# Performance work log

Measured on AMD Instinct MI355X. Metric: run time of the kernel, lower is better.

## Reference

```python
import jax, jax.numpy as jnp
import numpy as np

NUM_EMBEDDINGS = 1024
EMBEDDING_DIM = 64
COMMITMENT_COST = 0.25


def setup_inputs() -> dict:
    key = jax.random.key(0)
    k_in, k_w = jax.random.split(key)
    inputs = jax.random.normal(k_in, (32, 64, 32, 32), dtype=jnp.float32)
    # nn.Embedding weight initialized uniform(-1/K, 1/K)
    bound = 1.0 / NUM_EMBEDDINGS
    weight = jax.random.uniform(k_w, (NUM_EMBEDDINGS, EMBEDDING_DIM),
                                dtype=jnp.float32, minval=-bound, maxval=bound)
    return {"inputs": inputs, "weight": weight}


def reference(inputs, weight):
    # Flatten to [N, D] rows in embedding space
    flat = inputs.reshape(-1, EMBEDDING_DIM)  # [N, D]
    distances = (jnp.sum(flat * flat, axis=1, keepdims=True)
                 + jnp.sum(weight * weight, axis=1)
                 - 2.0 * jnp.matmul(flat, weight.T))
    encoding_indices = jnp.argmin(distances, axis=1)  # [N]
    quantized = weight[encoding_indices].reshape(inputs.shape)
    e_latent_loss = jnp.mean((jax.lax.stop_gradient(quantized) - inputs) ** 2)
    q_latent_loss = jnp.mean((quantized - jax.lax.stop_gradient(inputs)) ** 2)
    commitment_loss = COMMITMENT_COST * (q_latent_loss + e_latent_loss)
    # Straight-through estimator
    quantized = inputs + jax.lax.stop_gradient(quantized - inputs)
    return quantized, encoding_indices[:, None], commitment_loss
```

## Files before the change

kernel.cpp:

```cpp
#include <hip/hip_runtime.h>

#define NROWS  32768
#define DIM    64
#define KCODES 1024
#define NELEM  (NROWS * DIM)

__device__ __forceinline__ float np_sumsq64(const float v[64]) {
#pragma clang fp contract(off)
  float r0 = v[0] * v[0];
  float r1 = v[1] * v[1];
  float r2 = v[2] * v[2];
  float r3 = v[3] * v[3];
  float r4 = v[4] * v[4];
  float r5 = v[5] * v[5];
  float r6 = v[6] * v[6];
  float r7 = v[7] * v[7];
#pragma unroll
  for (int i = 8; i < 64; i += 8) {
    r0 += v[i + 0] * v[i + 0];
    r1 += v[i + 1] * v[i + 1];
    r2 += v[i + 2] * v[i + 2];
    r3 += v[i + 3] * v[i + 3];
    r4 += v[i + 4] * v[i + 4];
    r5 += v[i + 5] * v[i + 5];
    r6 += v[i + 6] * v[i + 6];
    r7 += v[i + 7] * v[i + 7];
  }
  return ((r0 + r1) + (r2 + r3)) + ((r4 + r5) + (r6 + r7));
}

__global__ void vq_prep(const float* __restrict__ w, float* __restrict__ se,
                        double* __restrict__ loss) {
  int c = blockIdx.x * 256 + threadIdx.x;
  if (c == 0) *loss = 0.0;
  if (c < KCODES) {
    float v[64];
    const float4* wr = (const float4*)(w + (size_t)c * DIM);
#pragma unroll
    for (int i = 0; i < 16; ++i) {
      float4 t = wr[i];
      v[4 * i + 0] = t.x; v[4 * i + 1] = t.y;
      v[4 * i + 2] = t.z; v[4 * i + 3] = t.w;
    }
    se[c] = np_sumsq64(v);
  }
}

__global__ __launch_bounds__(256) void vq_dist(const float* __restrict__ x,
                                               const float* __restrict__ w,
                                               const float* __restrict__ se,
                                               unsigned long long* __restrict__ keys) {
  const int g = blockIdx.x >> 2;
  const int chunk = blockIdx.x & 3;
  const int row = g * 256 + threadIdx.x;

  float xv[64];
  const float4* xr = (const float4*)(x + (size_t)row * DIM);
#pragma unroll
  for (int i = 0; i < 16; ++i) {
    float4 t = xr[i];
    xv[4 * i + 0] = t.x; xv[4 * i + 1] = t.y;
    xv[4 * i + 2] = t.z; xv[4 * i + 3] = t.w;
  }
  const float sx = np_sumsq64(xv);

  const int c0 = chunk * 256;
  const float4* w4 = (const float4*)w;
  unsigned long long best = 0xFFFFFFFFFFFFFFFFull;

#pragma unroll 2
  for (int j = 0; j < 256; ++j) {
    const int c = c0 + j;
    const float4* wr = w4 + (size_t)c * 16;
    float a0 = 0.f, a1 = 0.f, a2 = 0.f, a3 = 0.f;
#pragma unroll
    for (int i = 0; i < 16; ++i) {
      float4 t = wr[i];
      a0 += t.x * xv[4 * i + 0];
      a1 += t.y * xv[4 * i + 1];
      a2 += t.z * xv[4 * i + 2];
      a3 += t.w * xv[4 * i + 3];
    }
    float dot = (a0 + a1) + (a2 + a3);
    float ad = sx + se[c];
    float d  = ad - 2.0f * dot;
    unsigned long long key =
        ((unsigned long long)__float_as_uint(d) << 32) | (unsigned long long)c;
    if (key < best) best = key;
  }
  keys[(size_t)row * 4 + chunk] = best;
}

__global__ __launch_bounds__(256) void vq_out(const float* __restrict__ x,
                                              const float* __restrict__ w,
                                              const unsigned long long* __restrict__ keys,
                                              float* __restrict__ outq,
                                              float* __restrict__ outidx,
                                              double* __restrict__ loss) {
  __shared__ int sidx[256];
  __shared__ double red[256];
  const int b = blockIdx.x, t = threadIdx.x;
  const int row = b * 256 + t;

  const unsigned long long* kr = keys + (size_t)row * 4;
  unsigned long long k0 = kr[0], k1 = kr[1], k2 = kr[2], k3 = kr[3];
  unsigned long long kmin = k0 < k1 ? k0 : k1;
  unsigned long long kmin2 = k2 < k3 ? k2 : k3;
  if (kmin2 < kmin) kmin = kmin2;
  const int idx = (int)(kmin & 0xFFFFFFFFull);
  outidx[row] = (float)idx;
  sidx[t] = idx;
  __syncthreads();

  double acc = 0.0;
  const float4* x4 = (const float4*)x;
  float4* o4 = (float4*)outq;
#pragma unroll
  for (int i = 0; i < 16; ++i) {
    const int e  = i * 256 + t;
    const int rl = e >> 4;
    const int d4 = e & 15;
    const size_t gofs = (size_t)(b * 256 + rl) * 16 + d4;
    float4 xvv = x4[gofs];
    const float4* wr = (const float4*)(w + (size_t)sidx[rl] * DIM);
    float4 wv = wr[d4];
    float tx = wv.x - xvv.x, ty = wv.y - xvv.y;
    float tz = wv.z - xvv.z, tw = wv.w - xvv.w;
    float4 q;
    q.x = xvv.x + tx; q.y = xvv.y + ty;
    q.z = xvv.z + tz; q.w = xvv.w + tw;
    o4[gofs] = q;
    acc += (double)tx * tx + (double)ty * ty + (double)tz * tz + (double)tw * tw;
  }

  red[t] = acc;
  __syncthreads();
  for (int s = 128; s > 0; s >>= 1) {
    if (t < s) red[t] += red[t + s];
    __syncthreads();
  }
  if (t == 0) atomicAdd(loss, red[0]);
}

__global__ void vq_fin(const double* __restrict__ loss, float* __restrict__ outloss) {
  float m = (float)(*loss / (double)NELEM);
  *outloss = 0.5f * m;
}

extern "C" void kernel_launch(void* const* d_in, const int* in_sizes, int n_in,
                              void* d_out, int out_size, void* d_ws, size_t ws_size,
                              hipStream_t stream) {
  const float* x = (const float*)d_in[0];
  const float* w = (const float*)d_in[1];

  float* outq    = (float*)d_out;
  float* outidx  = outq + NELEM;
  float* outloss = outidx + NROWS;

  char* wsb = (char*)d_ws;
  double* loss = (double*)wsb;
  float* se = (float*)(wsb + 256);
  unsigned long long* keys = (unsigned long long*)(wsb + 8192);

  hipLaunchKernelGGL(vq_prep, dim3(4),   dim3(256), 0, stream, w, se, loss);
  hipLaunchKernelGGL(vq_dist, dim3(512), dim3(256), 0, stream, x, w, se, keys);
  hipLaunchKernelGGL(vq_out,  dim3(128), dim3(256), 0, stream, x, w, keys, outq, outidx, loss);
  hipLaunchKernelGGL(vq_fin,  dim3(1),   dim3(1),   0, stream, loss, outloss);
}
```

Before: 157.4 us.

## Split codebook into 8 chunks, pack FMAs as float2, merge keys via atomicMin

```diff
diff --git a/kernel.cpp b/kernel.cpp
--- a/kernel.cpp
+++ b/kernel.cpp
@@ -4,6 +4,8 @@
 #define DIM    64
 #define KCODES 1024
 #define NELEM  (NROWS * DIM)
+
+typedef float v2f __attribute__((ext_vector_type(2)));
 
 __device__ __forceinline__ float np_sumsq64(const float v[64]) {
 #pragma clang fp contract(off)
@@ -29,66 +31,87 @@
   return ((r0 + r1) + (r2 + r3)) + ((r4 + r5) + (r6 + r7));
 }
 
-__global__ void vq_prep(const float* __restrict__ w, float* __restrict__ se,
-                        double* __restrict__ loss) {
-  int c = blockIdx.x * 256 + threadIdx.x;
-  if (c == 0) *loss = 0.0;
-  if (c < KCODES) {
-    float v[64];
-    const float4* wr = (const float4*)(w + (size_t)c * DIM);
+__global__ __launch_bounds__(256) void vq_prep(const float* __restrict__ x,
+                                               const float* __restrict__ w,
+                                               float* __restrict__ se,
+                                               float* __restrict__ sxv,
+                                               unsigned long long* __restrict__ keys,
+                                               double* __restrict__ loss) {
+  const int t = blockIdx.x * 256 + threadIdx.x;
+  if (t == 0) *loss = 0.0;
+  keys[t] = ~0ull;
+
+  float v[64];
+  const float4* xr = (const float4*)(x + (size_t)t * DIM);
+#pragma unroll
+  for (int i = 0; i < 16; ++i) {
+    float4 q = xr[i];
+    v[4 * i + 0] = q.x; v[4 * i + 1] = q.y;
+    v[4 * i + 2] = q.z; v[4 * i + 3] = q.w;
+  }
+  sxv[t] = np_sumsq64(v);
+
+  if (t < KCODES) {
+    const float4* wr = (const float4*)(w + (size_t)t * DIM);
 #pragma unroll
     for (int i = 0; i < 16; ++i) {
-      float4 t = wr[i];
-      v[4 * i + 0] = t.x; v[4 * i + 1] = t.y;
-      v[4 * i + 2] = t.z; v[4 * i + 3] = t.w;
+      float4 q = wr[i];
+      v[4 * i + 0] = q.x; v[4 * i + 1] = q.y;
+      v[4 * i + 2] = q.z; v[4 * i + 3] = q.w;
     }
-    se[c] = np_sumsq64(v);
+    se[t] = np_sumsq64(v);
   }
 }
 
-__global__ __launch_bounds__(256) void vq_dist(const float* __restrict__ x,
-                                               const float* __restrict__ w,
-                                               const float* __restrict__ se,
-                                               unsigned long long* __restrict__ keys) {
-  const int g = blockIdx.x >> 2;
-  const int chunk = blockIdx.x & 3;
+__global__ __launch_bounds__(256, 4) void vq_dist(const float* __restrict__ x,
+                                                  const float* __restrict__ w,
+                                                  const float* __restrict__ se,
+                                                  const float* __restrict__ sxv,
+                                                  unsigned long long* __restrict__ keys) {
+  const int g = blockIdx.x >> 3;
+  const int chunk = blockIdx.x & 7;
   const int row = g * 256 + threadIdx.x;
 
-  float xv[64];
+  v2f xv[32];
   const float4* xr = (const float4*)(x + (size_t)row * DIM);
 #pragma unroll
   for (int i = 0; i < 16; ++i) {
     float4 t = xr[i];
-    xv[4 * i + 0] = t.x; xv[4 * i + 1] = t.y;
-    xv[4 * i + 2] = t.z; xv[4 * i + 3] = t.w;
+    xv[2 * i + 0] = (v2f){t.x, t.y};
+    xv[2 * i + 1] = (v2f){t.z, t.w};
   }
-  const float sx = np_sumsq64(xv);
+  const float sx = sxv[row];
 
-  const int c0 = chunk * 256;
+  const int c0 = chunk * 128;
   const float4* w4 = (const float4*)w;
-  unsigned long long best = 0xFFFFFFFFFFFFFFFFull;
+  unsigned long long best = ~0ull;
 
 #pragma unroll 2
-  for (int j = 0; j < 256; ++j) {
+  for (int j = 0; j < 128; ++j) {
     const int c = c0 + j;
     const float4* wr = w4 + (size_t)c * 16;
-    float a0 = 0.f, a1 = 0.f, a2 = 0.f, a3 = 0.f;
+    v2f a0 = (v2f){0.f, 0.f}, a1 = (v2f){0.f, 0.f};
+    v2f a2 = (v2f){0.f, 0.f}, a3 = (v2f){0.f, 0.f};
 #pragma unroll
-    for (int i = 0; i < 16; ++i) {
-      float4 t = wr[i];
-      a0 += t.x * xv[4 * i + 0];
-      a1 += t.y * xv[4 * i + 1];
-      a2 += t.z * xv[4 * i + 2];
-      a3 += t.w * xv[4 * i + 3];
+    for (int i = 0; i < 16; i += 2) {
+      float4 t0 = wr[i];
+      float4 t1 = wr[i + 1];
+      a0 += (v2f){t0.x, t0.y} * xv[2 * i + 0];
+      a1 += (v2f){t0.z, t0.w} * xv[2 * i + 1];
+      a2 += (v2f){t1.x, t1.y} * xv[2 * i + 2];
+      a3 += (v2f){t1.z, t1.w} * xv[2 * i + 3];
     }
-    float dot = (a0 + a1) + (a2 + a3);
+    v2f s01 = a0 + a1;
+    v2f s23 = a2 + a3;
+    v2f s = s01 + s23;
+    float dot = s.x + s.y;
     float ad = sx + se[c];
-    float d  = ad - 2.0f * dot;
+    float d = fmaf(-2.0f, dot, ad);
     unsigned long long key =
         ((unsigned long long)__float_as_uint(d) << 32) | (unsigned long long)c;
     if (key < best) best = key;
   }
-  keys[(size_t)row * 4 + chunk] = best;
+  atomicMin(&keys[row], best);
 }
 
 __global__ __launch_bounds__(256) void vq_out(const float* __restrict__ x,
@@ -97,30 +120,28 @@
                                               float* __restrict__ outq,
                                               float* __restrict__ outidx,
                                               double* __restrict__ loss) {
-  __shared__ int sidx[256];
-  __shared__ double red[256];
+  __shared__ int sidx[128];
+  __shared__ double part[4];
   const int b = blockIdx.x, t = threadIdx.x;
-  const int row = b * 256 + t;
 
-  const unsigned long long* kr = keys + (size_t)row * 4;
-  unsigned long long k0 = kr[0], k1 = kr[1], k2 = kr[2], k3 = kr[3];
-  unsigned long long kmin = k0 < k1 ? k0 : k1;
-  unsigned long long kmin2 = k2 < k3 ? k2 : k3;
-  if (kmin2 < kmin) kmin = kmin2;
-  const int idx = (int)(kmin & 0xFFFFFFFFull);
-  outidx[row] = (float)idx;
-  sidx[t] = idx;
+  if (t < 128) {
+    const int row = b * 128 + t;
+    unsigned long long k = keys[row];
+    const int idx = (int)(unsigned int)(k & 0xFFFFFFFFull);
+    outidx[row] = (float)idx;
+    sidx[t] = idx;
+  }
   __syncthreads();
 
   double acc = 0.0;
   const float4* x4 = (const float4*)x;
   float4* o4 = (float4*)outq;
 #pragma unroll
-  for (int i = 0; i < 16; ++i) {
-    const int e  = i * 256 + t;
+  for (int i = 0; i < 8; ++i) {
+    const int e = i * 256 + t;
     const int rl = e >> 4;
     const int d4 = e & 15;
-    const size_t gofs = (size_t)(b * 256 + rl) * 16 + d4;
+    const size_t gofs = ((size_t)b * 128 + rl) * 16 + d4;
     float4 xvv = x4[gofs];
     const float4* wr = (const float4*)(w + (size_t)sidx[rl] * DIM);
     float4 wv = wr[d4];
@@ -133,13 +154,11 @@
     acc += (double)tx * tx + (double)ty * ty + (double)tz * tz + (double)tw * tw;
   }
 
-  red[t] = acc;
+#pragma unroll
+  for (int s = 32; s > 0; s >>= 1) acc += __shfl_down(acc, s, 64);
+  if ((t & 63) == 0) part[t >> 6] = acc;
   __syncthreads();
-  for (int s = 128; s > 0; s >>= 1) {
-    if (t < s) red[t] += red[t + s];
-    __syncthreads();
-  }
-  if (t == 0) atomicAdd(loss, red[0]);
+  if (t == 0) atomicAdd(loss, (part[0] + part[1]) + (part[2] + part[3]));
 }
 
 __global__ void vq_fin(const double* __restrict__ loss, float* __restrict__ outloss) {
@@ -159,11 +178,12 @@
 
   char* wsb = (char*)d_ws;
   double* loss = (double*)wsb;
-  float* se = (float*)(wsb + 256);
-  unsigned long long* keys = (unsigned long long*)(wsb + 8192);
+  float* se    = (float*)(wsb + 256);
+  float* sxv   = (float*)(wsb + 8192);
+  unsigned long long* keys = (unsigned long long*)(wsb + 147456);
 
-  hipLaunchKernelGGL(vq_prep, dim3(4),   dim3(256), 0, stream, w, se, loss);
-  hipLaunchKernelGGL(vq_dist, dim3(512), dim3(256), 0, stream, x, w, se, keys);
-  hipLaunchKernelGGL(vq_out,  dim3(128), dim3(256), 0, stream, x, w, keys, outq, outidx, loss);
-  hipLaunchKernelGGL(vq_fin,  dim3(1),   dim3(1),   0, stream, loss, outloss);
+  hipLaunchKernelGGL(vq_prep, dim3(128),  dim3(256), 0, stream, x, w, se, sxv, keys, loss);
+  hipLaunchKernelGGL(vq_dist, dim3(1024), dim3(256), 0, stream, x, w, se, sxv, keys);
+  hipLaunchKernelGGL(vq_out,  dim3(256),  dim3(256), 0, stream, x, w, keys, outq, outidx, loss);
+  hipLaunchKernelGGL(vq_fin,  dim3(1),    dim3(1),   0, stream, loss, outloss);
 }
```

New measurement: 130.2 us. -17.3%, faster.

## Split each row across thread pairs, fuse codebook norms and loss finalization

Applied to the files above, without the earlier changes.

```diff
diff --git a/kernel.cpp b/kernel.cpp
--- a/kernel.cpp
+++ b/kernel.cpp
@@ -4,123 +4,121 @@
 #define DIM    64
 #define KCODES 1024
 #define NELEM  (NROWS * DIM)
+#define CHUNKS 4
+#define CPC    256
+#define RPB    128
+#define NBLK_B 256
 
-__device__ __forceinline__ float np_sumsq64(const float v[64]) {
+typedef float v2f __attribute__((ext_vector_type(2)));
+
+__device__ __forceinline__ float np_sumsq_f4(const float4* __restrict__ p) {
 #pragma clang fp contract(off)
-  float r0 = v[0] * v[0];
-  float r1 = v[1] * v[1];
-  float r2 = v[2] * v[2];
-  float r3 = v[3] * v[3];
-  float r4 = v[4] * v[4];
-  float r5 = v[5] * v[5];
-  float r6 = v[6] * v[6];
-  float r7 = v[7] * v[7];
+  float4 a = p[0], b = p[1];
+  float r0 = a.x * a.x, r1 = a.y * a.y, r2 = a.z * a.z, r3 = a.w * a.w;
+  float r4 = b.x * b.x, r5 = b.y * b.y, r6 = b.z * b.z, r7 = b.w * b.w;
 #pragma unroll
-  for (int i = 8; i < 64; i += 8) {
-    r0 += v[i + 0] * v[i + 0];
-    r1 += v[i + 1] * v[i + 1];
-    r2 += v[i + 2] * v[i + 2];
-    r3 += v[i + 3] * v[i + 3];
-    r4 += v[i + 4] * v[i + 4];
-    r5 += v[i + 5] * v[i + 5];
-    r6 += v[i + 6] * v[i + 6];
-    r7 += v[i + 7] * v[i + 7];
+  for (int i = 1; i < 8; ++i) {
+    a = p[2 * i]; b = p[2 * i + 1];
+    r0 += a.x * a.x; r1 += a.y * a.y; r2 += a.z * a.z; r3 += a.w * a.w;
+    r4 += b.x * b.x; r5 += b.y * b.y; r6 += b.z * b.z; r7 += b.w * b.w;
   }
   return ((r0 + r1) + (r2 + r3)) + ((r4 + r5) + (r6 + r7));
 }
 
-__global__ void vq_prep(const float* __restrict__ w, float* __restrict__ se,
-                        double* __restrict__ loss) {
-  int c = blockIdx.x * 256 + threadIdx.x;
-  if (c == 0) *loss = 0.0;
-  if (c < KCODES) {
-    float v[64];
-    const float4* wr = (const float4*)(w + (size_t)c * DIM);
-#pragma unroll
-    for (int i = 0; i < 16; ++i) {
-      float4 t = wr[i];
-      v[4 * i + 0] = t.x; v[4 * i + 1] = t.y;
-      v[4 * i + 2] = t.z; v[4 * i + 3] = t.w;
-    }
-    se[c] = np_sumsq64(v);
-  }
-}
-
-__global__ __launch_bounds__(256) void vq_dist(const float* __restrict__ x,
-                                               const float* __restrict__ w,
-                                               const float* __restrict__ se,
-                                               unsigned long long* __restrict__ keys) {
+__global__ __launch_bounds__(256, 4) void vq_dist(const float* __restrict__ x,
+                                                  const float* __restrict__ w,
+                                                  unsigned long long* __restrict__ keys4,
+                                                  double* __restrict__ loss,
+                                                  unsigned int* __restrict__ cnt) {
+  __shared__ float se[CPC];
+  const int t = threadIdx.x;
   const int g = blockIdx.x >> 2;
   const int chunk = blockIdx.x & 3;
-  const int row = g * 256 + threadIdx.x;
+  const int c0 = chunk * CPC;
 
-  float xv[64];
+  if (blockIdx.x == 0 && t == 0) { *loss = 0.0; *cnt = 0u; }
+
+  se[t] = np_sumsq_f4((const float4*)(w + (size_t)(c0 + t) * DIM));
+
+  const int row = g * RPB + (t >> 1);
+  const int half = t & 1;
   const float4* xr = (const float4*)(x + (size_t)row * DIM);
+
+  const float sx = np_sumsq_f4(xr);
+
+  v2f xv[16];
+  {
+    const float4* xh = xr + half * 8;
 #pragma unroll
-  for (int i = 0; i < 16; ++i) {
-    float4 t = xr[i];
-    xv[4 * i + 0] = t.x; xv[4 * i + 1] = t.y;
-    xv[4 * i + 2] = t.z; xv[4 * i + 3] = t.w;
+    for (int i = 0; i < 8; ++i) {
+      float4 q = xh[i];
+      xv[2 * i + 0] = (v2f){q.x, q.y};
+      xv[2 * i + 1] = (v2f){q.z, q.w};
+    }
   }
-  const float sx = np_sumsq64(xv);
+  __syncthreads();
 
-  const int c0 = chunk * 256;
-  const float4* w4 = (const float4*)w;
-  unsigned long long best = 0xFFFFFFFFFFFFFFFFull;
+  const float4* wbase = (const float4*)w;
+  float best_d = 3.4e38f;
+  int best_c = 0;
 
 #pragma unroll 2
-  for (int j = 0; j < 256; ++j) {
+  for (int j = 0; j < CPC; ++j) {
     const int c = c0 + j;
-    const float4* wr = w4 + (size_t)c * 16;
-    float a0 = 0.f, a1 = 0.f, a2 = 0.f, a3 = 0.f;
+    const float4* wr = wbase + ((size_t)c << 4) + (half << 3);
+    v2f acc = (v2f){0.f, 0.f};
 #pragma unroll
-    for (int i = 0; i < 16; ++i) {
-      float4 t = wr[i];
-      a0 += t.x * xv[4 * i + 0];
-      a1 += t.y * xv[4 * i + 1];
-      a2 += t.z * xv[4 * i + 2];
-      a3 += t.w * xv[4 * i + 3];
+    for (int i = 0; i < 8; ++i) {
+      float4 q = wr[i];
+      acc += (v2f){q.x, q.y} * xv[2 * i + 0];
+      acc += (v2f){q.z, q.w} * xv[2 * i + 1];
     }
-    float dot = (a0 + a1) + (a2 + a3);
-    float ad = sx + se[c];
-    float d  = ad - 2.0f * dot;
-    unsigned long long key =
-        ((unsigned long long)__float_as_uint(d) << 32) | (unsigned long long)c;
-    if (key < best) best = key;
+    float s = acc.x + acc.y;
+    float dot = s + __shfl_xor(s, 1, 64);
+    float ad = sx + se[j];
+    float d = fmaf(-2.0f, dot, ad);
+    if (d < best_d) { best_d = d; best_c = c; }
   }
-  keys[(size_t)row * 4 + chunk] = best;
+
+  unsigned long long key =
+      ((unsigned long long)__float_as_uint(best_d) << 32) | (unsigned int)best_c;
+  if (half == 0) keys4[((size_t)row << 2) | chunk] = key;
 }
 
 __global__ __launch_bounds__(256) void vq_out(const float* __restrict__ x,
                                               const float* __restrict__ w,
-                                              const unsigned long long* __restrict__ keys,
+                                              const unsigned long long* __restrict__ keys4,
                                               float* __restrict__ outq,
                                               float* __restrict__ outidx,
-                                              double* __restrict__ loss) {
-  __shared__ int sidx[256];
-  __shared__ double red[256];
+                                              double* __restrict__ loss,
+                                              unsigned int* __restrict__ cnt,
+                                              float* __restrict__ outloss) {
+  __shared__ int sidx[RPB];
+  __shared__ double part[4];
   const int b = blockIdx.x, t = threadIdx.x;
-  const int row = b * 256 + t;
 
-  const unsigned long long* kr = keys + (size_t)row * 4;
-  unsigned long long k0 = kr[0], k1 = kr[1], k2 = kr[2], k3 = kr[3];
-  unsigned long long kmin = k0 < k1 ? k0 : k1;
-  unsigned long long kmin2 = k2 < k3 ? k2 : k3;
-  if (kmin2 < kmin) kmin = kmin2;
-  const int idx = (int)(kmin & 0xFFFFFFFFull);
-  outidx[row] = (float)idx;
-  sidx[t] = idx;
+  if (t < RPB) {
+    const int row = b * RPB + t;
+    const unsigned long long* kr = keys4 + ((size_t)row << 2);
+    unsigned long long k0 = kr[0], k1 = kr[1], k2 = kr[2], k3 = kr[3];
+    unsigned long long ka = k0 < k1 ? k0 : k1;
+    unsigned long long kb = k2 < k3 ? k2 : k3;
+    unsigned long long k = ka < kb ? ka : kb;
+    const int idx = (int)(unsigned int)(k & 0xFFFFFFFFull);
+    outidx[row] = (float)idx;
+    sidx[t] = idx;
+  }
   __syncthreads();
 
   double acc = 0.0;
   const float4* x4 = (const float4*)x;
   float4* o4 = (float4*)outq;
 #pragma unroll
-  for (int i = 0; i < 16; ++i) {
-    const int e  = i * 256 + t;
+  for (int i = 0; i < 8; ++i) {
+    const int e = i * 256 + t;
     const int rl = e >> 4;
     const int d4 = e & 15;
-    const size_t gofs = (size_t)(b * 256 + rl) * 16 + d4;
+    const size_t gofs = ((size_t)b * RPB + rl) * 16 + d4;
     float4 xvv = x4[gofs];
     const float4* wr = (const float4*)(w + (size_t)sidx[rl] * DIM);
     float4 wv = wr[d4];
@@ -133,18 +131,19 @@
     acc += (double)tx * tx + (double)ty * ty + (double)tz * tz + (double)tw * tw;
   }
 
-  red[t] = acc;
+#pragma unroll
+  for (int s = 32; s > 0; s >>= 1) acc += __shfl_down(acc, s, 64);
+  if ((t & 63) == 0) part[t >> 6] = acc;
   __syncthreads();
-  for (int s = 128; s > 0; s >>= 1) {
-    if (t < s) red[t] += red[t + s];
-    __syncthreads();
+  if (t == 0) {
+    atomicAdd(loss, (part[0] + part[1]) + (part[2] + part[3]));
+    __threadfence();
+    unsigned int old = atomicAdd(cnt, 1u);
+    if (old == NBLK_B - 1) {
+      double L = atomicAdd(loss, 0.0);
+      *outloss = 0.5f * (float)(L / (double)NELEM);
+    }
   }
-  if (t == 0) atomicAdd(loss, red[0]);
-}
-
-__global__ void vq_fin(const double* __restrict__ loss, float* __restrict__ outloss) {
-  float m = (float)(*loss / (double)NELEM);
-  *outloss = 0.5f * m;
 }
 
 extern "C" void kernel_launch(void* const* d_in, const int* in_sizes, int n_in,
@@ -159,11 +158,11 @@
 
   char* wsb = (char*)d_ws;
   double* loss = (double*)wsb;
-  float* se = (float*)(wsb + 256);
-  unsigned long long* keys = (unsigned long long*)(wsb + 8192);
+  unsigned int* cnt = (unsigned int*)(wsb + 64);
+  unsigned long long* keys4 = (unsigned long long*)(wsb + 256);
 
-  hipLaunchKernelGGL(vq_prep, dim3(4),   dim3(256), 0, stream, w, se, loss);
-  hipLaunchKernelGGL(vq_dist, dim3(512), dim3(256), 0, stream, x, w, se, keys);
-  hipLaunchKernelGGL(vq_out,  dim3(128), dim3(256), 0, stream, x, w, keys, outq, outidx, loss);
-  hipLaunchKernelGGL(vq_fin,  dim3(1),   dim3(1),   0, stream, loss, outloss);
+  hipLaunchKernelGGL(vq_dist, dim3(1024),  dim3(256), 0, stream,
+                     x, w, keys4, loss, cnt);
+  hipLaunchKernelGGL(vq_out,  dim3(NBLK_B), dim3(256), 0, stream,
+                     x, w, keys4, outq, outidx, loss, cnt, outloss);
 }
```

After: 534.1 us. 239% more time.
